# Performance work log

Measured on AMD Instinct MI355X. Metric: run time of the kernel, lower is better.

The kernel has to match this reference:

```python
import jax, jax.numpy as jnp
import numpy as np

B, N, D_IN = 4, 2048, 1024
H, D_OUT = 8, 128


def setup_inputs() -> dict:
    key = jax.random.key(0)
    k1, k2, k3 = jax.random.split(key, 3)
    x = jax.random.normal(k1, (B, N, D_IN), dtype=jnp.float32)
    # W: (num_head, 3 [q,k,v], d_in, output_dim), glorot-ish scale
    W = jax.random.normal(k2, (H, 3, D_IN, D_OUT), dtype=jnp.float32) * (1.0 / np.sqrt(D_IN))
    Wo = jax.random.normal(k3, (H * D_OUT, D_OUT), dtype=jnp.float32) * (1.0 / np.sqrt(H * D_OUT))
    return {"x": x, "W": W, "Wo": Wo}


def reference(x, W, Wo):
    # Per-head QKV projections, vectorized over heads.
    # q,k,v: [B, H, N, D_OUT]
    q = jnp.einsum("bnd,hde->bhne", x, W[:, 0])
    k = jnp.einsum("bnd,hde->bhne", x, W[:, 1])
    v = jnp.einsum("bnd,hde->bhne", x, W[:, 2])
    scale = 1.0 / jnp.sqrt(jnp.asarray(D_OUT, dtype=x.dtype))
    # scores: [B, H, N, N]
    e = jnp.einsum("bhne,bhme->bhnm", q, k) * scale
    a = jax.nn.softmax(e, axis=-1)
    o = jnp.einsum("bhnm,bhme->bhne", a, v)  # [B, H, N, D_OUT]
    # concat heads -> [B, N, H*D_OUT]; head i occupies slice [i*D_OUT:(i+1)*D_OUT]
    o = jnp.transpose(o, (0, 2, 1, 3)).reshape(x.shape[0], x.shape[1], H * D_OUT)
    z = jnp.einsum("bnf,fe->bne", o, Wo)  # [B, N, D_OUT]
    return z
```

## Files before the change

### kernel.cpp

```cpp
#include <hip/hip_runtime.h>
#include <cstdint>


#define DEV __device__ __forceinline__

typedef _Float16 h8 __attribute__((ext_vector_type(8)));
typedef _Float16 h4 __attribute__((ext_vector_type(4)));
typedef float f4 __attribute__((ext_vector_type(4)));

typedef __attribute__((address_space(1))) const uint32_t gu32;
typedef __attribute__((address_space(3))) uint32_t lu32;

DEV float fexp2(float x) { return __builtin_amdgcn_exp2f(x); }

DEV f4 mfma16(h8 a, h8 b, f4 c) {
  return __builtin_amdgcn_mfma_f32_16x16x32_f16(a, b, c, 0, 0, 0);
}

DEV void g2l16(void* lds, const void* g) {
  __builtin_amdgcn_global_load_lds((gu32*)(uintptr_t)g, (lu32*)(uintptr_t)lds,
                                   16, 0, 0);
}

DEV f4 sx4(f4 v, int m) {
  f4 r;
  r[0] = __shfl_xor(v[0], m, 64);
  r[1] = __shfl_xor(v[1], m, 64);
  r[2] = __shfl_xor(v[2], m, 64);
  r[3] = __shfl_xor(v[3], m, 64);
  return r;
}

__global__ __launch_bounds__(256) void cvt_x_kernel(const float* __restrict__ x,
                                                    _Float16* __restrict__ Xb) {
  size_t i = (size_t)(blockIdx.x * 256 + threadIdx.x) * 4;
  f4 v = *(const f4*)(x + i);
  h4 o;
  o[0] = (_Float16)v[0];
  o[1] = (_Float16)v[1];
  o[2] = (_Float16)v[2];
  o[3] = (_Float16)v[3];
  *(h4*)(Xb + i) = o;
}

__global__ __launch_bounds__(256) void cvt_wt_kernel(const float* __restrict__ W,
                                                     const float* __restrict__ Wo,
                                                     _Float16* __restrict__ WT,
                                                     _Float16* __restrict__ WoT) {
  __shared__ float st[64][68];
  const int mz = blockIdx.z;
  const float* src = (mz < 24) ? (W + (size_t)mz * 131072) : Wo;
  _Float16* dst = (mz < 24) ? (WT + (size_t)mz * 131072) : WoT;
  const int d0 = blockIdx.x * 64;
  const int e0 = blockIdx.y * 64;
  const int tid = threadIdx.x;
#pragma unroll
  for (int r = 0; r < 4; ++r) {
    int idx = r * 256 + tid;
    int dd = idx >> 4, cc = (idx & 15) * 4;
    f4 v = *(const f4*)(src + (size_t)(d0 + dd) * 128 + e0 + cc);
    *(f4*)&st[dd][cc] = v;
  }
  __syncthreads();
#pragma unroll
  for (int r = 0; r < 2; ++r) {
    int idx = r * 256 + tid;
    int ee = idx >> 3, dd = (idx & 7) * 8;
    h8 o;
#pragma unroll
    for (int i = 0; i < 8; ++i) o[i] = (_Float16)st[dd + i][ee];
    *(h8*)(dst + (size_t)(e0 + ee) * 1024 + d0 + dd) = o;
  }
}

__global__ __launch_bounds__(256, 2) void gemm_qkv_kernel(
    const _Float16* __restrict__ A, const _Float16* __restrict__ BTall,
    _Float16* __restrict__ Qb, _Float16* __restrict__ Kb,
    _Float16* __restrict__ VTb) {
  constexpr int K = 1024;
  __shared__ __align__(16) _Float16 sAB[16384];
  const int tid = threadIdx.x;
  const int wave = tid >> 6, lane = tid & 63;
  const int g = lane >> 4, l15 = lane & 15;
  const int sw = l15 & 7;
  const int m0 = blockIdx.y * 128;
  const int j = blockIdx.x;
  const _Float16* BT = BTall + (size_t)j * (128 * 1024);

  f4 acc[4][4] = {};
  const int ar = (wave >> 1) * 64 + l15;
  const int br = (wave & 1) * 64 + l15;

#pragma unroll 1
  for (int kt = 0; kt < K; kt += 64) {
    __syncthreads();
#pragma unroll
    for (int r = 0; r < 4; ++r) {
      int idx = r * 256 + tid;
      int row = idx >> 3;
      int jg = (idx & 7) ^ (row & 7);
      g2l16(&sAB[idx * 8], A + (size_t)(m0 + row) * K + kt + jg * 8);
      g2l16(&sAB[8192 + idx * 8], BT + (size_t)row * K + kt + jg * 8);
    }
    __syncthreads();
#pragma unroll
    for (int ks = 0; ks < 2; ++ks) {
      int off = ((ks * 4 + g) ^ sw) * 8;
      h8 af[4], bf[4];
#pragma unroll
      for (int mt = 0; mt < 4; ++mt)
        af[mt] = *(const h8*)&sAB[(ar + mt * 16) * 64 + off];
#pragma unroll
      for (int nt = 0; nt < 4; ++nt)
        bf[nt] = *(const h8*)&sAB[8192 + (br + nt * 16) * 64 + off];
#pragma unroll
      for (int mt = 0; mt < 4; ++mt)
#pragma unroll
        for (int nt = 0; nt < 4; ++nt)
          acc[mt][nt] = mfma16(af[mt], bf[nt], acc[mt][nt]);
    }
  }

  const int wr = (wave >> 1) * 64, wc = (wave & 1) * 64;
  const int h = j / 3, s = j - h * 3;
  if (s < 2) {
    const float scl = (s == 0) ? 0.12751741032075984f : 1.0f;
    _Float16* dst = (s == 0) ? Qb : Kb;
    __syncthreads();
#pragma unroll
    for (int mt = 0; mt < 4; ++mt)
#pragma unroll
      for (int rg = 0; rg < 4; ++rg) {
        int rl = wr + mt * 16 + g * 4 + rg;
#pragma unroll
        for (int nt = 0; nt < 4; ++nt) {
          int c = wc + nt * 16 + l15;
          sAB[rl * 128 + (((c >> 3) ^ (rl & 7)) * 8) + (c & 7)] =
              (_Float16)(acc[mt][nt][rg] * scl);
        }
      }
    __syncthreads();
    int rr = tid >> 1, seg = tid & 1;
    int m = m0 + rr, b = m >> 11, n = m & 2047;
    size_t rb = ((size_t)((b * 8 + h) * 2048 + n)) * 128;
#pragma unroll
    for (int k = 0; k < 8; ++k) {
      int ch = seg * 8 + k;
      h8 v = *(const h8*)&sAB[rr * 128 + ((ch ^ (rr & 7)) * 8)];
      *(h8*)&dst[rb + ch * 8] = v;
    }
  } else {
    __syncthreads();
    const int b = m0 >> 11, n0 = m0 & 2047;
    size_t base = (size_t)(b * 8 + h) * (128 * 2048);
#pragma unroll
    for (int mt = 0; mt < 4; ++mt)
#pragma unroll
      for (int rg = 0; rg < 4; ++rg) {
        int nl = wr + mt * 16 + g * 4 + rg;
        int cc = (nl >> 3), ci = nl & 7;
#pragma unroll
        for (int nt = 0; nt < 4; ++nt) {
          int c = wc + nt * 16 + l15;
          sAB[c * 128 + ((cc ^ (c & 7)) * 8) + ci] = (_Float16)acc[mt][nt][rg];
        }
      }
    __syncthreads();
    int c = tid >> 1, seg = tid & 1;
#pragma unroll
    for (int k = 0; k < 8; ++k) {
      int ch = seg * 8 + k;
      h8 v = *(const h8*)&sAB[c * 128 + ((ch ^ (c & 7)) * 8)];
      *(h8*)&VTb[base + (size_t)c * 2048 + n0 + ch * 8] = v;
    }
  }
}

__global__ __launch_bounds__(256, 4) void flash_kernel(
    const _Float16* __restrict__ Qb, const _Float16* __restrict__ Kb,
    const _Float16* __restrict__ VTb, _Float16* __restrict__ Oc) {
  __shared__ __align__(16) _Float16 sK[64 * 128];
  __shared__ __align__(16) _Float16 sVT[128 * 64];
  __shared__ __align__(16) _Float16 sP[4 * 16 * 64];
  const int tid = threadIdx.x, wave = tid >> 6, lane = tid & 63;
  const int g = lane >> 4, l15 = lane & 15;
  const int sw = l15 & 7;
  const int bh = blockIdx.x, b = bh >> 3, h = bh & 7;
  const int q0 = blockIdx.y * 64;
  const _Float16* Q = Qb + (size_t)bh * (2048 * 128);
  const _Float16* Kp = Kb + (size_t)bh * (2048 * 128);
  const _Float16* VT = VTb + (size_t)bh * (128 * 2048);
  _Float16* sPw = &sP[wave * (16 * 64)];

  h8 qf[4];
#pragma unroll
  for (int kk = 0; kk < 4; ++kk)
    qf[kk] = *(const h8*)&Q[(size_t)(q0 + wave * 16 + l15) * 128 + kk * 32 + g * 8];

  f4 oacc[8] = {};
  f4 lstate = {};

#pragma unroll 1
  for (int kv0 = 0; kv0 < 2048; kv0 += 64) {
    __syncthreads();
#pragma unroll
    for (int r = 0; r < 4; ++r) {
      int idx = r * 256 + tid;
      int row = idx >> 4;
      int jg = (idx & 15) ^ (row & 7);
      g2l16(&sK[idx * 8], Kp + (size_t)(kv0 + row) * 128 + jg * 8);
      int row2 = idx >> 3;
      int jg2 = (idx & 7) ^ (row2 & 7);
      g2l16(&sVT[idx * 8], VT + (size_t)row2 * 2048 + kv0 + jg2 * 8);
    }
    __syncthreads();

    f4 sacc[4] = {};
#pragma unroll
    for (int kk = 0; kk < 4; ++kk) {
      int off = ((kk * 4 + g) ^ sw) * 8;
#pragma unroll
      for (int nt = 0; nt < 4; ++nt) {
        h8 bf = *(const h8*)&sK[(nt * 16 + l15) * 128 + off];
        sacc[nt] = mfma16(qf[kk], bf, sacc[nt]);
      }
    }

#pragma unroll
    for (int nt = 0; nt < 4; ++nt) {
      f4 p;
      p[0] = fexp2(sacc[nt][0]);
      p[1] = fexp2(sacc[nt][1]);
      p[2] = fexp2(sacc[nt][2]);
      p[3] = fexp2(sacc[nt][3]);
      lstate += p;
      int cc = nt * 2 + (l15 >> 3), ci = l15 & 7;
#pragma unroll
      for (int rg = 0; rg < 4; ++rg) {
        int rl = g * 4 + rg;
        sPw[rl * 64 + ((cc ^ (rl & 7)) * 8) + ci] = (_Float16)p[rg];
      }
    }

#pragma unroll
    for (int kk = 0; kk < 2; ++kk) {
      int off = ((kk * 4 + g) ^ sw) * 8;
      h8 pa = *(const h8*)&sPw[l15 * 64 + off];
#pragma unroll
      for (int nt = 0; nt < 8; ++nt) {
        h8 vb = *(const h8*)&sVT[(nt * 16 + l15) * 64 + off];
        oacc[nt] = mfma16(pa, vb, oacc[nt]);
      }
    }
  }

#pragma unroll
  for (int d = 1; d < 16; d <<= 1) lstate += sx4(lstate, d);
  f4 inv;
  inv[0] = 1.0f / lstate[0];
  inv[1] = 1.0f / lstate[1];
  inv[2] = 1.0f / lstate[2];
  inv[3] = 1.0f / lstate[3];
#pragma unroll
  for (int rg = 0; rg < 4; ++rg) {
    int n = q0 + wave * 16 + g * 4 + rg;
    size_t rb = ((size_t)(b * 2048 + n)) * 1024 + h * 128;
#pragma unroll
    for (int nt = 0; nt < 8; ++nt)
      Oc[rb + nt * 16 + l15] = (_Float16)(oacc[nt][rg] * inv[rg]);
  }
}

__global__ __launch_bounds__(256, 2) void gemm_out_kernel(
    const _Float16* __restrict__ A, const _Float16* __restrict__ BT,
    float* __restrict__ outF) {
  __shared__ __align__(16) _Float16 sA[32 * 64];
  __shared__ __align__(16) _Float16 sB[128 * 64];
  const int tid = threadIdx.x, wave = tid >> 6, lane = tid & 63;
  const int g = lane >> 4, l15 = lane & 15, sw = l15 & 7;
  const int m0 = blockIdx.x * 32;
  f4 acc[2][2] = {};

#pragma unroll 1
  for (int kt = 0; kt < 1024; kt += 64) {
    __syncthreads();
    {
      int row = tid >> 3;
      int jg = (tid & 7) ^ (row & 7);
      g2l16(&sA[tid * 8], A + (size_t)(m0 + row) * 1024 + kt + jg * 8);
    }
#pragma unroll
    for (int r = 0; r < 4; ++r) {
      int idx = r * 256 + tid;
      int row = idx >> 3;
      int jg = (idx & 7) ^ (row & 7);
      g2l16(&sB[idx * 8], BT + (size_t)row * 1024 + kt + jg * 8);
    }
    __syncthreads();
#pragma unroll
    for (int ks = 0; ks < 2; ++ks) {
      int off = ((ks * 4 + g) ^ sw) * 8;
      h8 af[2], bf[2];
#pragma unroll
      for (int mt = 0; mt < 2; ++mt)
        af[mt] = *(const h8*)&sA[(mt * 16 + l15) * 64 + off];
#pragma unroll
      for (int nt = 0; nt < 2; ++nt)
        bf[nt] = *(const h8*)&sB[(wave * 32 + nt * 16 + l15) * 64 + off];
#pragma unroll
      for (int mt = 0; mt < 2; ++mt)
#pragma unroll
        for (int nt = 0; nt < 2; ++nt)
          acc[mt][nt] = mfma16(af[mt], bf[nt], acc[mt][nt]);
    }
  }
#pragma unroll
  for (int mt = 0; mt < 2; ++mt)
#pragma unroll
    for (int rg = 0; rg < 4; ++rg) {
      int m = m0 + mt * 16 + g * 4 + rg;
#pragma unroll
      for (int nt = 0; nt < 2; ++nt)
        outF[(size_t)m * 128 + wave * 32 + nt * 16 + l15] = acc[mt][nt][rg];
    }
}

extern "C" void kernel_launch(void* const* d_in, const int* in_sizes, int n_in,
                              void* d_out, int out_size, void* d_ws,
                              size_t ws_size, hipStream_t stream) {
  const float* x = (const float*)d_in[0];
  const float* W = (const float*)d_in[1];
  const float* Wo = (const float*)d_in[2];
  float* out = (float*)d_out;
  char* ws = (char*)d_ws;

  _Float16* Xb = (_Float16*)(ws + 0);
  _Float16* WT = (_Float16*)(ws + 16777216);
  _Float16* WoT = (_Float16*)(ws + 23068672);
  _Float16* Qb = (_Float16*)(ws + 23330816);
  _Float16* Kb = (_Float16*)(ws + 40108032);
  _Float16* VTb = (_Float16*)(ws + 56885248);
  _Float16* Oc = (_Float16*)(ws + 73662464);

  cvt_x_kernel<<<8192, 256, 0, stream>>>(x, Xb);
  cvt_wt_kernel<<<dim3(16, 2, 25), 256, 0, stream>>>(W, Wo, WT, WoT);
  gemm_qkv_kernel<<<dim3(24, 64), 256, 0, stream>>>(Xb, WT, Qb, Kb, VTb);
  flash_kernel<<<dim3(32, 32), 256, 0, stream>>>(Qb, Kb, VTb, Oc);
  gemm_out_kernel<<<256, 256, 0, stream>>>(Oc, WoT, out);
}
```

Baseline: 277.0 us.

## Reuse K tile LDS for P, swap QKV grid order, shrink output GEMM tiles

Flash attention now stores the P tile in the K tile's LDS buffer, with an extra barrier after the QK^T MFMAs, so shared memory per block shrinks and more blocks may fit. The QKV GEMM swaps its grid axes so consecutive blocks walk M for the same weight slice, and raises its occupancy hint from 2 to 3. The output GEMM halves its M tile to 16 rows, doubling the block count to fill more CUs, with occupancy hint 4. The cost is an extra barrier per KV tile and less reuse of the Wo tile in the output GEMM.

```diff
diff --git a/kernel.cpp b/kernel.cpp
--- a/kernel.cpp
+++ b/kernel.cpp
@@ -73,7 +73,7 @@
   }
 }
 
-__global__ __launch_bounds__(256, 2) void gemm_qkv_kernel(
+__global__ __launch_bounds__(256, 3) void gemm_qkv_kernel(
     const _Float16* __restrict__ A, const _Float16* __restrict__ BTall,
     _Float16* __restrict__ Qb, _Float16* __restrict__ Kb,
     _Float16* __restrict__ VTb) {
@@ -83,8 +83,8 @@
   const int wave = tid >> 6, lane = tid & 63;
   const int g = lane >> 4, l15 = lane & 15;
   const int sw = l15 & 7;
-  const int m0 = blockIdx.y * 128;
-  const int j = blockIdx.x;
+  const int m0 = blockIdx.x * 128;
+  const int j = blockIdx.y;
   const _Float16* BT = BTall + (size_t)j * (128 * 1024);
 
   f4 acc[4][4] = {};
@@ -181,7 +181,6 @@
     const _Float16* __restrict__ VTb, _Float16* __restrict__ Oc) {
   __shared__ __align__(16) _Float16 sK[64 * 128];
   __shared__ __align__(16) _Float16 sVT[128 * 64];
-  __shared__ __align__(16) _Float16 sP[4 * 16 * 64];
   const int tid = threadIdx.x, wave = tid >> 6, lane = tid & 63;
   const int g = lane >> 4, l15 = lane & 15;
   const int sw = l15 & 7;
@@ -190,7 +189,7 @@
   const _Float16* Q = Qb + (size_t)bh * (2048 * 128);
   const _Float16* Kp = Kb + (size_t)bh * (2048 * 128);
   const _Float16* VT = VTb + (size_t)bh * (128 * 2048);
-  _Float16* sPw = &sP[wave * (16 * 64)];
+  _Float16* sPw = &sK[wave * (16 * 64)];
 
   h8 qf[4];
 #pragma unroll
@@ -225,6 +224,7 @@
         sacc[nt] = mfma16(qf[kk], bf, sacc[nt]);
       }
     }
+    __syncthreads();
 
 #pragma unroll
     for (int nt = 0; nt < 4; ++nt) {
@@ -271,20 +271,20 @@
   }
 }
 
-__global__ __launch_bounds__(256, 2) void gemm_out_kernel(
+__global__ __launch_bounds__(256, 4) void gemm_out_kernel(
     const _Float16* __restrict__ A, const _Float16* __restrict__ BT,
     float* __restrict__ outF) {
-  __shared__ __align__(16) _Float16 sA[32 * 64];
+  __shared__ __align__(16) _Float16 sA[16 * 64];
   __shared__ __align__(16) _Float16 sB[128 * 64];
   const int tid = threadIdx.x, wave = tid >> 6, lane = tid & 63;
   const int g = lane >> 4, l15 = lane & 15, sw = l15 & 7;
-  const int m0 = blockIdx.x * 32;
-  f4 acc[2][2] = {};
+  const int m0 = blockIdx.x * 16;
+  f4 acc[2] = {};
 
 #pragma unroll 1
   for (int kt = 0; kt < 1024; kt += 64) {
     __syncthreads();
-    {
+    if (tid < 128) {
       int row = tid >> 3;
       int jg = (tid & 7) ^ (row & 7);
       g2l16(&sA[tid * 8], A + (size_t)(m0 + row) * 1024 + kt + jg * 8);
@@ -300,29 +300,21 @@
 #pragma unroll
     for (int ks = 0; ks < 2; ++ks) {
       int off = ((ks * 4 + g) ^ sw) * 8;
-      h8 af[2], bf[2];
-#pragma unroll
-      for (int mt = 0; mt < 2; ++mt)
-        af[mt] = *(const h8*)&sA[(mt * 16 + l15) * 64 + off];
-#pragma unroll
-      for (int nt = 0; nt < 2; ++nt)
-        bf[nt] = *(const h8*)&sB[(wave * 32 + nt * 16 + l15) * 64 + off];
-#pragma unroll
-      for (int mt = 0; mt < 2; ++mt)
-#pragma unroll
-        for (int nt = 0; nt < 2; ++nt)
-          acc[mt][nt] = mfma16(af[mt], bf[nt], acc[mt][nt]);
-    }
-  }
-#pragma unroll
-  for (int mt = 0; mt < 2; ++mt)
-#pragma unroll
-    for (int rg = 0; rg < 4; ++rg) {
-      int m = m0 + mt * 16 + g * 4 + rg;
-#pragma unroll
-      for (int nt = 0; nt < 2; ++nt)
-        outF[(size_t)m * 128 + wave * 32 + nt * 16 + l15] = acc[mt][nt][rg];
-    }
+      h8 af = *(const h8*)&sA[l15 * 64 + off];
+#pragma unroll
+      for (int nt = 0; nt < 2; ++nt) {
+        h8 bf = *(const h8*)&sB[(wave * 32 + nt * 16 + l15) * 64 + off];
+        acc[nt] = mfma16(af, bf, acc[nt]);
+      }
+    }
+  }
+#pragma unroll
+  for (int rg = 0; rg < 4; ++rg) {
+    int m = m0 + g * 4 + rg;
+#pragma unroll
+    for (int nt = 0; nt < 2; ++nt)
+      outF[(size_t)m * 128 + wave * 32 + nt * 16 + l15] = acc[nt][rg];
+  }
 }
 
 extern "C" void kernel_launch(void* const* d_in, const int* in_sizes, int n_in,
@@ -344,7 +336,7 @@
 
   cvt_x_kernel<<<8192, 256, 0, stream>>>(x, Xb);
   cvt_wt_kernel<<<dim3(16, 2, 25), 256, 0, stream>>>(W, Wo, WT, WoT);
-  gemm_qkv_kernel<<<dim3(24, 64), 256, 0, stream>>>(Xb, WT, Qb, Kb, VTb);
+  gemm_qkv_kernel<<<dim3(64, 24), 256, 0, stream>>>(Xb, WT, Qb, Kb, VTb);
   flash_kernel<<<dim3(32, 32), 256, 0, stream>>>(Qb, Kb, VTb, Oc);
-  gemm_out_kernel<<<256, 256, 0, stream>>>(Oc, WoT, out);
-}
+  gemm_out_kernel<<<512, 256, 0, stream>>>(Oc, WoT, out);
+}
```

Result: no change. 277.3 us (+0.1%).
